# Performance work log

Measured on AMD Instinct MI355X. Metric: run time of the kernel, lower is better.

## Reference

```python
import jax, jax.numpy as jnp
import numpy as np

N, C, A = 1024, 200, 256
P, Q, EPS = 0.8, 2.0, 0.01  # cls_Loss defaults


def setup_inputs() -> dict:
    key = jax.random.key(0)
    ks = jax.random.split(key, 7)
    return {
        "fc_weight": jax.random.normal(ks[0], (C, A), jnp.float32) * 0.05,
        "features_source": jax.random.normal(ks[1], (N, A), jnp.float32),
        "y_s": jax.random.normal(ks[2], (N, C), jnp.float32),
        "labels_source": jax.random.randint(ks[3], (N,), 0, C),
        "Lambda": jnp.float32(0.5),
        "mean_source": jax.random.normal(ks[4], (C, A), jnp.float32),
        "mean_target": jax.random.normal(ks[5], (C, A), jnp.float32),
        "covariance_target": jax.random.normal(ks[6], (C, A, A), jnp.float32) * 0.01,
    }


def _aug(fc_weight, y_s, labels, Lambda, mean_s, mean_t, cov_t):
    # D[n,c,:] = W[c] - W[labels[n]]   (NxW_ij - NxW_kj)
    D = fc_weight[None, :, :] - fc_weight[labels][:, None, :]  # [N,C,A]
    CVn = cov_t[labels]                                        # [N,A,A]
    # diagonal of D @ CV @ D^T computed directly (no NxCxC intermediate)
    M = jnp.einsum('nab,ncb->nca', CVn, D)                     # [N,C,A]
    sigma2 = Lambda * jnp.sum(D * M, axis=-1)                  # [N,C]
    dmean = mean_t[labels] - mean_s[labels]                    # [N,A]
    shift = jnp.einsum('nca,na->nc', D, dmean)                 # [N,C]
    return y_s + 0.5 * sigma2 + Lambda * shift


def _cls_loss(outputs, targets):
    n = outputs.shape[0]
    # accumulated starts at zero buffer -> equals per-class counts of this batch
    counts = jnp.zeros((C,), jnp.float32).at[targets].add(1.0)
    acc = jnp.maximum(counts, 1.0)
    matrix = acc[None, :] / acc[:, None]                       # [C,C]
    sample_w = jnp.where(matrix < 1.0, matrix ** P, 1.0)
    mitigation = sample_w[targets]                             # [N,C]
    scores = jax.nn.softmax(jax.lax.stop_gradient(outputs), axis=1)
    self_scores = scores[jnp.arange(n), targets]               # [N]
    score_matrix = scores / jnp.maximum(self_scores, EPS)[:, None]
    compensation = jnp.where(score_matrix > 1.0, score_matrix ** Q, 1.0)
    seesaw = mitigation * compensation                         # [N,C]
    onehot = jax.nn.one_hot(targets, C, dtype=outputs.dtype)
    logits = outputs + jnp.log(seesaw) * (1.0 - onehot)
    logp = jax.nn.log_softmax(logits, axis=1)
    nll = -jnp.take_along_axis(logp, targets[:, None], axis=1)[:, 0]
    return jnp.mean(nll)


def reference(fc_weight, features_source, y_s, labels_source, Lambda,
              mean_source, mean_target, covariance_target):
    # features_source only provides N, A in the original; not used numerically
    aug_y = _aug(fc_weight, y_s, labels_source, Lambda,
                 mean_source, mean_target, covariance_target)
    return _cls_loss(aug_y, labels_source)
```

## Files before the change

kernel.cpp:

```cpp
#include <hip/hip_runtime.h>
#include <hip/hip_fp16.h>
#include <math.h>

#define NN 1024
#define CC 200
#define AA 256

static constexpr float P_EXP = 0.8f;
static constexpr float Q_EXP = 2.0f;
static constexpr float EPS_C = 0.01f;

typedef __attribute__((ext_vector_type(8))) _Float16 half8;
typedef __attribute__((ext_vector_type(4))) _Float16 half4v;
typedef __attribute__((ext_vector_type(4))) float f32x4;

__global__ void k_prep(const float* __restrict__ W, const int* __restrict__ lab,
                       _Float16* __restrict__ Whf, float* __restrict__ accv){
  if (blockIdx.x == 52){
    __shared__ int cnt[CC];
    int t = threadIdx.x;
    for (int i = t; i < CC; i += 256) cnt[i] = 0;
    __syncthreads();
    for (int n = t; n < NN; n += 256) atomicAdd(&cnt[lab[n]], 1);
    __syncthreads();
    for (int i = t; i < CC; i += 256) accv[i] = fmaxf((float)cnt[i], 1.0f);
    return;
  }
  int idx = (blockIdx.x * 256 + threadIdx.x) * 4;
  if (idx >= 208 * AA) return;
  float4 w = make_float4(0.f, 0.f, 0.f, 0.f);
  if (idx < CC * AA) w = *(const float4*)(W + idx);
  Whf[idx + 0] = (_Float16)w.x;
  Whf[idx + 1] = (_Float16)w.y;
  Whf[idx + 2] = (_Float16)w.z;
  Whf[idx + 3] = (_Float16)w.w;
}

__global__ __launch_bounds__(512) void k_quad(
    const _Float16* __restrict__ Whf, const float* __restrict__ CV,
    const float* __restrict__ ms, const float* __restrict__ mtg,
    const float* __restrict__ lamp, float* __restrict__ tbl)
{
  const int q    = blockIdx.x;
  const int l    = blockIdx.y;
  const int tid  = threadIdx.x;
  const int wid  = tid >> 6;
  const int lane = tid & 63;
  const int lrow = lane & 15;
  const int kgrp = lane >> 4;

  __shared__ float4 cvb[2][16][64];
  __shared__ _Float16 dmh[64];

  if (tid < 64)
    dmh[tid] = (_Float16)(2.f * (mtg[l * AA + q * 64 + tid] - ms[l * AA + q * 64 + tid]));

  const int ct0 = wid, ct1 = wid + 8;
  half8 ef0[8], ef1[8];
  #pragma unroll
  for (int kt = 0; kt < 8; ++kt){
    half8 wlv = *(const half8*)(Whf + l * AA + kt * 32 + kgrp * 8);
    half8 wc0 = *(const half8*)(Whf + (ct0 * 16 + lrow) * AA + kt * 32 + kgrp * 8);
    ef0[kt] = wc0 - wlv;
    if (wid < 5){
      half8 wc1 = *(const half8*)(Whf + (ct1 * 16 + lrow) * AA + kt * 32 + kgrp * 8);
      ef1[kt] = wc1 - wlv;
    }
  }

  const size_t cvbase = (size_t)l * AA * AA + (size_t)q * 64 * AA;

  #define STAGE(TILE, BUF) do {                                               \
    _Pragma("unroll")                                                         \
    for (int rr_ = 0; rr_ < 2; ++rr_){                                        \
      int row_ = wid * 2 + rr_;                                               \
      const float* gs_ = CV + cvbase + (size_t)(TILE) * 16 * AA               \
                       + (size_t)row_ * AA + ((lane ^ (row_ & 7)) << 2);      \
      __builtin_amdgcn_global_load_lds(                                       \
        (const __attribute__((address_space(1))) void*)gs_,                   \
        (__attribute__((address_space(3))) void*)&cvb[BUF][row_][0],          \
        16, 0, 0);                                                            \
    }                                                                         \
  } while(0)

  STAGE(0, 0);
  __syncthreads();

  f32x4 D2a = {0.f,0.f,0.f,0.f}, D2b = {0.f,0.f,0.f,0.f};
  const float lam = lamp[0];

  for (int t = 0; t < 4; ++t){
    if (t + 1 < 4) STAGE(t + 1, (t + 1) & 1);

    const int buf = t & 1;
    f32x4 a0 = {0.f,0.f,0.f,0.f}, a1 = {0.f,0.f,0.f,0.f};
    #pragma unroll
    for (int kt = 0; kt < 8; ++kt){
      const int j0 = kt * 8 + kgrp * 2;
      float4 v0 = cvb[buf][lrow][( j0     ) ^ (lrow & 7)];
      float4 v1 = cvb[buf][lrow][( j0 + 1 ) ^ (lrow & 7)];
      half8 cvf;
      cvf[0]=(_Float16)v0.x; cvf[1]=(_Float16)v0.y; cvf[2]=(_Float16)v0.z; cvf[3]=(_Float16)v0.w;
      cvf[4]=(_Float16)v1.x; cvf[5]=(_Float16)v1.y; cvf[6]=(_Float16)v1.z; cvf[7]=(_Float16)v1.w;
      a0 = __builtin_amdgcn_mfma_f32_16x16x32_f16(cvf, ef0[kt], a0, 0, 0, 0);
      if (wid < 5)
        a1 = __builtin_amdgcn_mfma_f32_16x16x32_f16(cvf, ef1[kt], a1, 0, 0, 0);
    }

    const int aslg = q * 64 + t * 16 + kgrp * 4;
    half4v wl2 = *(const half4v*)(Whf + l * AA + aslg);
    half4v dmf = *(const half4v*)&dmh[t * 16 + kgrp * 4];
    {
      half4v wc2 = *(const half4v*)(Whf + (ct0 * 16 + lrow) * AA + aslg);
      half4v e2  = wc2 - wl2;
      half4v b2;
      b2[0]=(_Float16)a0[0]; b2[1]=(_Float16)a0[1]; b2[2]=(_Float16)a0[2]; b2[3]=(_Float16)a0[3];
      D2a = __builtin_amdgcn_mfma_f32_16x16x16f16(e2, b2,  D2a, 0, 0, 0);
      D2a = __builtin_amdgcn_mfma_f32_16x16x16f16(e2, dmf, D2a, 0, 0, 0);
    }
    if (wid < 5){
      half4v wc2 = *(const half4v*)(Whf + (ct1 * 16 + lrow) * AA + aslg);
      half4v e2  = wc2 - wl2;
      half4v b2;
      b2[0]=(_Float16)a1[0]; b2[1]=(_Float16)a1[1]; b2[2]=(_Float16)a1[2]; b2[3]=(_Float16)a1[3];
      D2b = __builtin_amdgcn_mfma_f32_16x16x16f16(e2, b2,  D2b, 0, 0, 0);
      D2b = __builtin_amdgcn_mfma_f32_16x16x16f16(e2, dmf, D2b, 0, 0, 0);
    }

    __syncthreads();
  }

  if ((lrow >> 2) == kgrp){
    const int jj = lrow & 3;
    const int c0 = ct0 * 16 + lrow;
    float d0 = (jj == 0) ? D2a[0] : (jj == 1) ? D2a[1] : (jj == 2) ? D2a[2] : D2a[3];
    if (c0 < CC) tbl[(size_t)q * CC * CC + l * CC + c0] = 0.5f * lam * d0;
    if (wid < 5){
      const int c1 = ct1 * 16 + lrow;
      float d1 = (jj == 0) ? D2b[0] : (jj == 1) ? D2b[1] : (jj == 2) ? D2b[2] : D2b[3];
      if (c1 < CC) tbl[(size_t)q * CC * CC + l * CC + c1] = 0.5f * lam * d1;
    }
  }
  #undef STAGE
}

__global__ __launch_bounds__(64) void k_rows(
    const float* __restrict__ ys, const int* __restrict__ lab,
    const float* __restrict__ accv, const float* __restrict__ tbl,
    float* __restrict__ nll)
{
  const int n    = blockIdx.x;
  const int lane = threadIdx.x;
  const int l    = lab[n];
  const float acc_l = accv[l];
  const float log_acc_l = logf(acc_l);

  float z[4];
  float m = -1e30f;
  #pragma unroll
  for (int k = 0; k < 4; k++){
    int cidx = k * 64 + lane;
    float zz = -1e30f;
    if (cidx < CC){
      zz = ys[n * CC + cidx]
         + tbl[              l * CC + cidx] + tbl[    CC * CC + l * CC + cidx]
         + tbl[2 * CC * CC + l * CC + cidx] + tbl[3 * CC * CC + l * CC + cidx];
    }
    z[k] = zz;
    m = fmaxf(m, zz);
  }
  for (int o = 32; o; o >>= 1) m = fmaxf(m, __shfl_xor(m, o));

  float se = 0.f;
  #pragma unroll
  for (int k = 0; k < 4; k++){
    int cidx = k * 64 + lane;
    if (cidx < CC) se += expf(z[k] - m);
  }
  for (int o = 32; o; o >>= 1) se += __shfl_xor(se, o);
  const float L0 = m + logf(se);

  const int kl = l >> 6, ll = l & 63;
  float zsel = (kl == 0) ? z[0] : (kl == 1 ? z[1] : (kl == 2 ? z[2] : z[3]));
  const float zl = __shfl(zsel, ll);
  const float logden = fmaxf(zl - L0, logf(EPS_C));

  float lg[4];
  float m2 = -1e30f;
  #pragma unroll
  for (int k = 0; k < 4; k++){
    int cidx = k * 64 + lane;
    float lz = -1e30f;
    if (cidx < CC){
      lz = z[k];
      if (cidx != l){
        float lratio = (z[k] - L0) - logden;
        float lcomp  = (lratio > 0.f) ? Q_EXP * lratio : 0.f;
        float accc   = accv[cidx];
        float lmit   = (accc < acc_l) ? P_EXP * (logf(accc) - log_acc_l) : 0.f;
        lz += lcomp + lmit;
      }
    }
    lg[k] = lz;
    m2 = fmaxf(m2, lz);
  }
  for (int o = 32; o; o >>= 1) m2 = fmaxf(m2, __shfl_xor(m2, o));
  float se2 = 0.f;
  #pragma unroll
  for (int k = 0; k < 4; k++){
    int cidx = k * 64 + lane;
    if (cidx < CC) se2 += expf(lg[k] - m2);
  }
  for (int o = 32; o; o >>= 1) se2 += __shfl_xor(se2, o);
  const float L1 = m2 + logf(se2);

  if (lane == 0) nll[n] = L1 - zl;
}

__global__ void k_mean(const float* __restrict__ nll, float* __restrict__ out){
  __shared__ float s[256];
  int t = threadIdx.x;
  float v = 0.f;
  for (int i = t; i < NN; i += 256) v += nll[i];
  s[t] = v; __syncthreads();
  for (int o = 128; o; o >>= 1){ if (t < o) s[t] += s[t + o]; __syncthreads(); }
  if (t == 0) out[0] = s[0] / (float)NN;
}

extern "C" void kernel_launch(void* const* d_in, const int* in_sizes, int n_in,
                              void* d_out, int out_size, void* d_ws, size_t ws_size,
                              hipStream_t stream) {
  const float* W   = (const float*)d_in[0];
  const float* ys  = (const float*)d_in[2];
  const int*   lab = (const int*)  d_in[3];
  const float* lam = (const float*)d_in[4];
  const float* ms  = (const float*)d_in[5];
  const float* mt  = (const float*)d_in[6];
  const float* CV  = (const float*)d_in[7];

  float* ws   = (float*)d_ws;
  float* tbl  = ws;
  float* accv = ws + 160000;
  float* nll  = ws + 160256;
  _Float16* Whf = (_Float16*)(ws + 161280);
  float* out  = (float*)d_out;

  k_prep <<<53, 256, 0, stream>>>(W, lab, Whf, accv);
  dim3 gq(4, CC);
  k_quad <<<gq, 512, 0, stream>>>(Whf, CV, ms, mt, lam, tbl);
  k_rows <<<NN, 64, 0, stream>>>(ys, lab, accv, tbl, nll);
  k_mean <<<1, 256, 0, stream>>>(nll, out);
}
```

Baseline: 56.81 us.

## Load covariance slab once into fp16 LDS, drop double-buffered pipeline

Each block now loads its whole 64x256 covariance slab into registers with vectorized global loads, converts it to fp16 once and stores it into a swizzled LDS array. This replaces the 4-stage double-buffered global_load_lds pipeline and the per-tile fp32-to-fp16 conversion in the MFMA loop. It also removes the per-tile barriers and computes the mean delta directly from global memory instead of through shared memory. The intent is fewer conversions and syncs, at the cost of more registers, 32KB of LDS per block and no overlap between the load and compute phases.

```diff
diff --git a/kernel.cpp b/kernel.cpp
--- a/kernel.cpp
+++ b/kernel.cpp
@@ -49,11 +49,13 @@
   const int lrow = lane & 15;
   const int kgrp = lane >> 4;
 
-  __shared__ float4 cvb[2][16][64];
-  __shared__ _Float16 dmh[64];
-
-  if (tid < 64)
-    dmh[tid] = (_Float16)(2.f * (mtg[l * AA + q * 64 + tid] - ms[l * AA + q * 64 + tid]));
+  __shared__ _Float16 cvh[64][256];
+
+  const float* src = CV + (size_t)l * AA * AA + (size_t)q * 64 * AA;
+  float4 v[8];
+  #pragma unroll
+  for (int i = 0; i < 8; ++i)
+    v[i] = *(const float4*)(src + (size_t)(i * 512 + tid) * 4);
 
   const int ct0 = wid, ct1 = wid + 8;
   half8 ef0[8], ef1[8];
@@ -68,40 +70,29 @@
     }
   }
 
-  const size_t cvbase = (size_t)l * AA * AA + (size_t)q * 64 * AA;
-
-  #define STAGE(TILE, BUF) do {                                               \
-    _Pragma("unroll")                                                         \
-    for (int rr_ = 0; rr_ < 2; ++rr_){                                        \
-      int row_ = wid * 2 + rr_;                                               \
-      const float* gs_ = CV + cvbase + (size_t)(TILE) * 16 * AA               \
-                       + (size_t)row_ * AA + ((lane ^ (row_ & 7)) << 2);      \
-      __builtin_amdgcn_global_load_lds(                                       \
-        (const __attribute__((address_space(1))) void*)gs_,                   \
-        (__attribute__((address_space(3))) void*)&cvb[BUF][row_][0],          \
-        16, 0, 0);                                                            \
-    }                                                                         \
-  } while(0)
-
-  STAGE(0, 0);
+  #pragma unroll
+  for (int i = 0; i < 8; ++i){
+    int f    = i * 512 + tid;
+    int row  = f >> 6;
+    int c16  = f & 63;
+    int slot = (c16 >> 1) ^ (row & 7);
+    half4v h;
+    h[0] = (_Float16)v[i].x; h[1] = (_Float16)v[i].y;
+    h[2] = (_Float16)v[i].z; h[3] = (_Float16)v[i].w;
+    *(half4v*)(&cvh[row][0] + slot * 8 + (c16 & 1) * 4) = h;
+  }
   __syncthreads();
 
   f32x4 D2a = {0.f,0.f,0.f,0.f}, D2b = {0.f,0.f,0.f,0.f};
   const float lam = lamp[0];
 
+  #pragma unroll
   for (int t = 0; t < 4; ++t){
-    if (t + 1 < 4) STAGE(t + 1, (t + 1) & 1);
-
-    const int buf = t & 1;
     f32x4 a0 = {0.f,0.f,0.f,0.f}, a1 = {0.f,0.f,0.f,0.f};
+    const int row = t * 16 + lrow;
     #pragma unroll
     for (int kt = 0; kt < 8; ++kt){
-      const int j0 = kt * 8 + kgrp * 2;
-      float4 v0 = cvb[buf][lrow][( j0     ) ^ (lrow & 7)];
-      float4 v1 = cvb[buf][lrow][( j0 + 1 ) ^ (lrow & 7)];
-      half8 cvf;
-      cvf[0]=(_Float16)v0.x; cvf[1]=(_Float16)v0.y; cvf[2]=(_Float16)v0.z; cvf[3]=(_Float16)v0.w;
-      cvf[4]=(_Float16)v1.x; cvf[5]=(_Float16)v1.y; cvf[6]=(_Float16)v1.z; cvf[7]=(_Float16)v1.w;
+      half8 cvf = *(const half8*)(&cvh[row][0] + (((kt * 4 + kgrp) ^ (row & 7)) * 8));
       a0 = __builtin_amdgcn_mfma_f32_16x16x32_f16(cvf, ef0[kt], a0, 0, 0, 0);
       if (wid < 5)
         a1 = __builtin_amdgcn_mfma_f32_16x16x32_f16(cvf, ef1[kt], a1, 0, 0, 0);
@@ -109,7 +100,13 @@
 
     const int aslg = q * 64 + t * 16 + kgrp * 4;
     half4v wl2 = *(const half4v*)(Whf + l * AA + aslg);
-    half4v dmf = *(const half4v*)&dmh[t * 16 + kgrp * 4];
+    float4 dmt = *(const float4*)(mtg + l * AA + aslg);
+    float4 dms = *(const float4*)(ms  + l * AA + aslg);
+    half4v dmf;
+    dmf[0] = (_Float16)(2.f * (dmt.x - dms.x));
+    dmf[1] = (_Float16)(2.f * (dmt.y - dms.y));
+    dmf[2] = (_Float16)(2.f * (dmt.z - dms.z));
+    dmf[3] = (_Float16)(2.f * (dmt.w - dms.w));
     {
       half4v wc2 = *(const half4v*)(Whf + (ct0 * 16 + lrow) * AA + aslg);
       half4v e2  = wc2 - wl2;
@@ -126,8 +123,6 @@
       D2b = __builtin_amdgcn_mfma_f32_16x16x16f16(e2, b2,  D2b, 0, 0, 0);
       D2b = __builtin_amdgcn_mfma_f32_16x16x16f16(e2, dmf, D2b, 0, 0, 0);
     }
-
-    __syncthreads();
   }
 
   if ((lrow >> 2) == kgrp){
@@ -141,7 +136,6 @@
       if (c1 < CC) tbl[(size_t)q * CC * CC + l * CC + c1] = 0.5f * lam * d1;
     }
   }
-  #undef STAGE
 }
 
 __global__ __launch_bounds__(64) void k_rows(
```

After: 54.13 us. 4.7% less time.
